# Optimization experiments

Measured on AMD Instinct MI355X. Metric: run time of the kernel, lower is better.

Reference implementation:

```python
import jax, jax.numpy as jnp
import numpy as np


def setup_inputs() -> dict:
    key = jax.random.key(0)
    k1, k2, k3 = jax.random.split(key, 3)
    B, N, C, K = 4, 8192, 256, 16
    q = jax.random.normal(k1, (B, N, C), dtype=jnp.float32)
    q_pos = jax.random.normal(k2, (B, N, 3), dtype=jnp.float32)
    W = jax.random.normal(k3, (2 * C, C), dtype=jnp.float32) / np.sqrt(2 * C)
    b = jnp.zeros((C,), dtype=jnp.float32)
    return {"q": q, "q_pos": q_pos, "W": W, "b": b, "k": K}


def _square_distance(src, dst):
    # src [B,N,3], dst [B,M,3] -> [B,N,M]
    d = -2.0 * jnp.einsum("bnc,bmc->bnm", src, dst)
    d = d + jnp.sum(src * src, axis=-1)[:, :, None]
    d = d + jnp.sum(dst * dst, axis=-1)[:, None, :]
    return d


def reference(q, q_pos, W, b, k):
    # self-attention path: v = q, v_pos = q_pos
    v, v_pos = q, q_pos
    sqrdists = _square_distance(q_pos, v_pos)           # [B,N,M]
    _, idx = jax.lax.top_k(-sqrdists, k)                # k smallest -> [B,N,k]
    # gather neighbors: local_v[b,n,j] = v[b, idx[b,n,j]]
    local_v = jax.vmap(lambda vv, ii: vv[ii])(v, idx)   # [B,N,k,C]
    qk = jnp.broadcast_to(q[:, :, None, :], local_v.shape)
    feature = jnp.concatenate([local_v - qk, qk], axis=-1)  # [B,N,k,2C]
    h = jnp.einsum("bnkf,fc->bnkc", feature, W) + b
    h = jax.nn.leaky_relu(h, negative_slope=0.2)
    out = jnp.max(h, axis=-2)                           # [B,N,C]
    return out
```

## Files before the change

kernel.cpp:

```cpp
#include <hip/hip_runtime.h>
#include <hip/hip_bf16.h>
#include <cstdint>
#include <cstddef>

#define BATCH 4
#define NPT   8192
#define CH    256
#define KNN   16
#define BN_TOT (BATCH * NPT)
#define NSLICE 16
#define SLICE  (NPT / NSLICE)
#define CAP    32
#define MINI   32

typedef __attribute__((ext_vector_type(8))) short bf16x8;
typedef __attribute__((ext_vector_type(4))) float f32x4;

__device__ __forceinline__ float dist2np(const float4 qp, const float4 cp) {
#pragma clang fp contract(off)
  float acc = qp.x * cp.x;
  acc = __builtin_fmaf(qp.y, cp.y, acc);
  acc = __builtin_fmaf(qp.z, cp.z, acc);
  float t = -2.0f * acc;
  t = t + qp.w;
  t = t + cp.w;
  return t;
}

__device__ __forceinline__ unsigned int pk_bf16(float a, float b) {
  __hip_bfloat162 h = __float22bfloat162_rn(make_float2(a, b));
  return *(unsigned int*)&h;
}

__global__ __launch_bounds__(256) void prep_kernel(
    const float* __restrict__ q_pos, const float* __restrict__ W,
    float4* __restrict__ cpack, unsigned short* __restrict__ WbT)
{
  int t = blockIdx.x * 256 + threadIdx.x;
  {
    int k = t >> 9;
    int j = t & 511;
    float v;
    if (j < 256) {
      v = W[k * 256 + j];
    } else {
      int c = j - 256;
      v = W[(256 + k) * 256 + c] - W[k * 256 + c];
    }
    __hip_bfloat16 hb = __float2bfloat16(v);
    WbT[(size_t)j * 256 + k] = *(unsigned short*)&hb;
  }
  if (t < BN_TOT) {
#pragma clang fp contract(off)
    float x = q_pos[3 * t + 0];
    float y = q_pos[3 * t + 1];
    float z = q_pos[3 * t + 2];
    float px = x * x;
    float py = y * y;
    float pz = z * z;
    float s = px + py;
    s = s + pz;
    cpack[t] = make_float4(x, y, z, s);
  }
}

__global__ __launch_bounds__(1024, 8) void knn_kernel(
    const float4* __restrict__ cpack,
    int* __restrict__ idxout)
{
  __shared__ __align__(16) unsigned short cand[NSLICE * 64 * CAP];
  __shared__ unsigned int hist[32][64];
  __shared__ unsigned short scnt[NSLICE][64];
  __shared__ float edge_s[64];
  __shared__ int ubnd[64];

  const int tid = threadIdx.x;
  const int l   = tid & 63;
  const int w   = __builtin_amdgcn_readfirstlane(tid >> 6);
  const int b   = blockIdx.y;
  const int q   = b * NPT + blockIdx.x * 64 + l;

  ((unsigned int*)hist)[tid] = 0u;
  ((unsigned int*)hist)[tid + 1024] = 0u;
  __syncthreads();

  const float4 qp = cpack[q];
  const float m2x = -2.0f * qp.x, m2y = -2.0f * qp.y, m2z = -2.0f * qp.z;
  const float4* __restrict__ cb = cpack + b * NPT;
  const int m0 = w * SLICE;
  unsigned int* hb = (unsigned int*)((char*)&hist[0][0] - (241 << 8)) + l;

#pragma unroll 4
  for (int m = m0; m < m0 + MINI; ++m) {
    float4 cp = cb[m];
    float d = fmaf(m2z, cp.z, fmaf(m2y, cp.y, fmaf(m2x, cp.x, qp.w + cp.w)));
    int r = __float_as_int(d) >> 22;
    r = min(max(r, 241), 272);
    atomicAdd(hb + (r << 6), 1u);
  }
  __syncthreads();

  if (tid < 64) {
    int cum = 0, Bm = 31;
#pragma unroll 1
    for (int bb = 0; bb < 32; ++bb) {
      cum += (int)hist[bb][tid];
      if (cum >= KNN) { Bm = bb; break; }
    }
    ubnd[tid] = 241 + Bm;
  }
  __syncthreads();

  const int ub = ubnd[l];
  const float ubEdgef = __uint_as_float((unsigned)(ub + 1) << 22);
#pragma unroll 8
  for (int m = m0 + MINI; m < m0 + SLICE; ++m) {
    float4 cp = cb[m];
    float d = fmaf(m2z, cp.z, fmaf(m2y, cp.y, fmaf(m2x, cp.x, qp.w + cp.w)));
    if (d < ubEdgef) {
      int r = max(__float_as_int(d) >> 22, 241);
      atomicAdd(hb + (r << 6), 1u);
    }
  }
  __syncthreads();

  if (tid < 64) {
    int cum = 0, B = 31;
#pragma unroll 1
    for (int bb = 0; bb < 32; ++bb) {
      cum += (int)hist[bb][tid];
      if (cum >= KNN) { B = bb; break; }
    }
    edge_s[tid] = __uint_as_float((unsigned)(242 + B) << 22);
  }
  __syncthreads();

  const float edgef = edge_s[l];
  unsigned int cnt = 0;
  unsigned short* mybuf = &cand[(w * 64 + l) * CAP];
#pragma unroll 8
  for (int m = m0; m < m0 + SLICE; ++m) {
    float4 cp = cb[m];
    float d = fmaf(m2z, cp.z, fmaf(m2y, cp.y, fmaf(m2x, cp.x, qp.w + cp.w)));
    if (d < edgef) {
      if (cnt < CAP) mybuf[cnt] = (unsigned short)m;
      cnt++;
    }
  }
  scnt[w][l] = (unsigned short)(cnt < (unsigned)CAP ? cnt : (unsigned)CAP);
  __syncthreads();

  if ((tid >> 6) < 4) {
    const int g = tid >> 6;
    const int nself = (q & (NPT - 1));
    float rd[16]; int ri[16];
#pragma unroll
    for (int j = 0; j < 16; ++j) { rd[j] = __builtin_inff(); ri[j] = nself; }
#pragma unroll 1
    for (int w2 = 4 * g; w2 < 4 * g + 4; ++w2) {
      int cw = (int)scnt[w2][l];
      for (int i = 0; i < cw; ++i) {
        int m = (int)cand[(w2 * 64 + l) * CAP + i];
        float d = dist2np(qp, cb[m]);
        if (d < rd[15]) {
#pragma unroll
          for (int j = 15; j > 0; --j) {
            bool up = d < rd[j - 1];
            float nd = up ? rd[j - 1] : d;
            int   ni = up ? ri[j - 1] : m;
            if (d < rd[j]) { rd[j] = nd; ri[j] = ni; }
          }
          if (d < rd[0]) { rd[0] = d; ri[0] = m; }
        }
      }
    }
    float2* pls = (float2*)(cand + (size_t)g * 8192);
#pragma unroll
    for (int j = 0; j < 16; ++j) {
      int pos = (j + l) & 15;
      pls[l * 16 + pos] = make_float2(rd[j], __int_as_float(ri[j]));
    }
  }
  __syncthreads();

  if (tid < 64) {
    const float2* pls0 = (const float2*)(cand);
    const float2* pls1 = (const float2*)(cand + 8192);
    const float2* pls2 = (const float2*)(cand + 16384);
    const float2* pls3 = (const float2*)(cand + 24576);
    int p0 = 0, p1 = 0, p2 = 0, p3 = 0;
    float2 h0 = pls0[l * 16 + (l & 15)];
    float2 h1 = pls1[l * 16 + (l & 15)];
    float2 h2 = pls2[l * 16 + (l & 15)];
    float2 h3 = pls3[l * 16 + (l & 15)];
#pragma unroll 1
    for (int s = 0; s < 16; ++s) {
      float bd = h0.x; int be = __float_as_int(h0.y); int bg = 0;
      if (h1.x < bd) { bd = h1.x; be = __float_as_int(h1.y); bg = 1; }
      if (h2.x < bd) { bd = h2.x; be = __float_as_int(h2.y); bg = 2; }
      if (h3.x < bd) { bd = h3.x; be = __float_as_int(h3.y); bg = 3; }
      idxout[(size_t)q * 16 + s] = be;
      p0 += (bg == 0); p1 += (bg == 1); p2 += (bg == 2); p3 += (bg == 3);
      int q0 = p0 < 16 ? p0 : 15;
      int q1 = p1 < 16 ? p1 : 15;
      int q2 = p2 < 16 ? p2 : 15;
      int q3 = p3 < 16 ? p3 : 15;
      h0 = pls0[l * 16 + ((q0 + l) & 15)];
      h1 = pls1[l * 16 + ((q1 + l) & 15)];
      h2 = pls2[l * 16 + ((q2 + l) & 15)];
      h3 = pls3[l * 16 + ((q3 + l) & 15)];
    }
  }
}

#define ASTRIDE 40
__global__ __launch_bounds__(256) void gemm_kernel(
    const float* __restrict__ Q, const unsigned short* __restrict__ WbT,
    const float* __restrict__ bias,
    unsigned short* __restrict__ A16, float* __restrict__ Qn)
{
  __shared__ __align__(16) unsigned short As[128 * ASTRIDE];
  __shared__ __align__(16) unsigned short Bs[128 * ASTRIDE];
  const int tid  = threadIdx.x;
  const int lane = tid & 63;
  const int wv   = tid >> 6;
  const int wr   = wv & 1, wc = wv >> 1;
  const int bid  = blockIdx.x;
  const int bm0  = (bid >> 2) * 128;
  const int bn0  = (bid & 3) * 128;
  const int srow = tid >> 1;
  const int skh  = tid & 1;
  const int quad = lane >> 4;
  const int l15  = lane & 15;

  f32x4 acc[4][4];
#pragma unroll
  for (int i = 0; i < 4; ++i)
#pragma unroll
    for (int j = 0; j < 4; ++j) acc[i][j] = (f32x4)0.0f;

  const float* ag = Q + (size_t)(bm0 + srow) * 256 + skh * 16;
  const unsigned short* bg = WbT + (size_t)(bn0 + srow) * 256 + skh * 16;
  unsigned short* asw = &As[srow * ASTRIDE + skh * 16];
  unsigned short* bsw = &Bs[srow * ASTRIDE + skh * 16];

  for (int k0 = 0; k0 < 256; k0 += 32) {
    float4 f0 = *(const float4*)(ag + k0);
    float4 f1 = *(const float4*)(ag + k0 + 4);
    float4 f2 = *(const float4*)(ag + k0 + 8);
    float4 f3 = *(const float4*)(ag + k0 + 12);
    uint4 bv0 = *(const uint4*)(bg + k0);
    uint4 bv1 = *(const uint4*)(bg + k0 + 8);
    uint4 a0, a1;
    a0.x = pk_bf16(f0.x, f0.y); a0.y = pk_bf16(f0.z, f0.w);
    a0.z = pk_bf16(f1.x, f1.y); a0.w = pk_bf16(f1.z, f1.w);
    a1.x = pk_bf16(f2.x, f2.y); a1.y = pk_bf16(f2.z, f2.w);
    a1.z = pk_bf16(f3.x, f3.y); a1.w = pk_bf16(f3.z, f3.w);
    __syncthreads();
    *(uint4*)(asw) = a0;
    *(uint4*)(asw + 8) = a1;
    *(uint4*)(bsw) = bv0;
    *(uint4*)(bsw + 8) = bv1;
    __syncthreads();

    bf16x8 af[4], bf[4];
#pragma unroll
    for (int rt = 0; rt < 4; ++rt)
      af[rt] = *(const bf16x8*)&As[(wr * 64 + rt * 16 + l15) * ASTRIDE + quad * 8];
#pragma unroll
    for (int ct = 0; ct < 4; ++ct)
      bf[ct] = *(const bf16x8*)&Bs[(wc * 64 + ct * 16 + l15) * ASTRIDE + quad * 8];
#pragma unroll
    for (int rt = 0; rt < 4; ++rt)
#pragma unroll
      for (int ct = 0; ct < 4; ++ct)
        acc[rt][ct] = __builtin_amdgcn_mfma_f32_16x16x32_bf16(af[rt], bf[ct], acc[rt][ct], 0, 0, 0);
  }

  if (bn0 < 256) {
#pragma unroll
    for (int ct = 0; ct < 4; ++ct) {
      int col = bn0 + wc * 64 + ct * 16 + l15;
#pragma unroll
      for (int rt = 0; rt < 4; ++rt) {
        int rowb = bm0 + wr * 64 + rt * 16 + quad * 4;
#pragma unroll
        for (int r = 0; r < 4; ++r) {
          __hip_bfloat16 hb = __float2bfloat16(acc[rt][ct][r]);
          A16[(size_t)(rowb + r) * 256 + col] = *(unsigned short*)&hb;
        }
      }
    }
  } else {
#pragma unroll
    for (int ct = 0; ct < 4; ++ct) {
      int col = bn0 + wc * 64 + ct * 16 + l15 - 256;
      float bvl = bias[col];
#pragma unroll
      for (int rt = 0; rt < 4; ++rt) {
        int rowb = bm0 + wr * 64 + rt * 16 + quad * 4;
#pragma unroll
        for (int r = 0; r < 4; ++r)
          Qn[(size_t)(rowb + r) * 256 + col] = acc[rt][ct][r] + bvl;
      }
    }
  }
}

__global__ __launch_bounds__(256) void gather_kernel(
    const unsigned short* __restrict__ A16, const int* __restrict__ idxout,
    float* __restrict__ Out)
{
  __shared__ int sidx[16];
  const int q = blockIdx.x;
  const int b = q >> 13;
  const int c = threadIdx.x;
  if (c < 16) sidx[c] = idxout[(size_t)q * 16 + c];
  __syncthreads();
  const float qn = Out[(size_t)q * 256 + c];
  const unsigned short* __restrict__ Ab = A16 + (size_t)b * NPT * 256;
  float best = -__builtin_inff();
#pragma unroll
  for (int j = 0; j < 16; ++j) {
    unsigned short raw = Ab[(size_t)sidx[j] * 256 + c];
    float a = __uint_as_float((unsigned)raw << 16);
    float h = a + qn;
    best = fmaxf(best, fmaxf(h, 0.2f * h));
  }
  Out[(size_t)q * 256 + c] = best;
}

extern "C" void kernel_launch(void* const* d_in, const int* in_sizes, int n_in,
                              void* d_out, int out_size, void* d_ws, size_t ws_size,
                              hipStream_t stream)
{
  (void)in_sizes; (void)n_in; (void)out_size; (void)ws_size;
  const float* qf   = (const float*)d_in[0];
  const float* qpos = (const float*)d_in[1];
  const float* W    = (const float*)d_in[2];
  const float* bias = (const float*)d_in[3];

  char* ws = (char*)d_ws;
  size_t off = 0;
  auto alloc = [&](size_t bytes) {
    void* p = ws + off;
    off += (bytes + 255) & ~(size_t)255;
    return p;
  };
  float4* cpack       = (float4*)alloc((size_t)BN_TOT * sizeof(float4));
  unsigned short* WbT = (unsigned short*)alloc((size_t)512 * 256 * 2);
  int* idxout         = (int*)alloc((size_t)BN_TOT * KNN * sizeof(int));
  unsigned short* A16 = (unsigned short*)alloc((size_t)BN_TOT * CH * 2);
  float* Out          = (float*)d_out;

  prep_kernel<<<512, 256, 0, stream>>>(qpos, W, cpack, WbT);
  knn_kernel<<<dim3(128, BATCH), 1024, 0, stream>>>(cpack, idxout);
  gemm_kernel<<<1024, 256, 0, stream>>>(qf, WbT, bias, A16, Out);
  gather_kernel<<<BN_TOT, 256, 0, stream>>>(A16, idxout, Out);
}
```

Baseline: 288.4 us.

## Collect KNN candidates during histogram pass and vectorize neighbor gather

The KNN kernel now records candidate indices below the coarse upper bound while it builds the histogram. The third full scan of the slice then runs only when that buffer overflowed. This drops one pass over the slice in the common case, at the cost of extra buffer writes in the second pass. Separately, the gather kernel handles four queries per block and loads four channels per thread with ushort4/float4, which cuts the block count and the number of memory transactions.

```diff
diff --git a/kernel.cpp b/kernel.cpp
--- a/kernel.cpp
+++ b/kernel.cpp
@@ -113,11 +113,24 @@
 
   const int ub = ubnd[l];
   const float ubEdgef = __uint_as_float((unsigned)(ub + 1) << 22);
-#pragma unroll 8
+  unsigned int cnt = 0;
+  unsigned short* mybuf = &cand[(w * 64 + l) * CAP];
+#pragma unroll 4
+  for (int m = m0; m < m0 + MINI; ++m) {
+    float4 cp = cb[m];
+    float d = fmaf(m2z, cp.z, fmaf(m2y, cp.y, fmaf(m2x, cp.x, qp.w + cp.w)));
+    if (d < ubEdgef) {
+      if (cnt < CAP) mybuf[cnt] = (unsigned short)m;
+      cnt++;
+    }
+  }
+#pragma unroll 4
   for (int m = m0 + MINI; m < m0 + SLICE; ++m) {
     float4 cp = cb[m];
     float d = fmaf(m2z, cp.z, fmaf(m2y, cp.y, fmaf(m2x, cp.x, qp.w + cp.w)));
     if (d < ubEdgef) {
+      if (cnt < CAP) mybuf[cnt] = (unsigned short)m;
+      cnt++;
       int r = max(__float_as_int(d) >> 22, 241);
       atomicAdd(hb + (r << 6), 1u);
     }
@@ -135,16 +148,17 @@
   }
   __syncthreads();
 
-  const float edgef = edge_s[l];
-  unsigned int cnt = 0;
-  unsigned short* mybuf = &cand[(w * 64 + l) * CAP];
-#pragma unroll 8
-  for (int m = m0; m < m0 + SLICE; ++m) {
-    float4 cp = cb[m];
-    float d = fmaf(m2z, cp.z, fmaf(m2y, cp.y, fmaf(m2x, cp.x, qp.w + cp.w)));
-    if (d < edgef) {
-      if (cnt < CAP) mybuf[cnt] = (unsigned short)m;
-      cnt++;
+  if (cnt > (unsigned)CAP) {
+    const float edgef = edge_s[l];
+    cnt = 0;
+#pragma unroll 2
+    for (int m = m0; m < m0 + SLICE; ++m) {
+      float4 cp = cb[m];
+      float d = fmaf(m2z, cp.z, fmaf(m2y, cp.y, fmaf(m2x, cp.x, qp.w + cp.w)));
+      if (d < edgef) {
+        if (cnt < CAP) mybuf[cnt] = (unsigned short)m;
+        cnt++;
+      }
     }
   }
   scnt[w][l] = (unsigned short)(cnt < (unsigned)CAP ? cnt : (unsigned)CAP);
@@ -311,23 +325,35 @@
     const unsigned short* __restrict__ A16, const int* __restrict__ idxout,
     float* __restrict__ Out)
 {
-  __shared__ int sidx[16];
-  const int q = blockIdx.x;
-  const int b = q >> 13;
-  const int c = threadIdx.x;
-  if (c < 16) sidx[c] = idxout[(size_t)q * 16 + c];
-  __syncthreads();
-  const float qn = Out[(size_t)q * 256 + c];
-  const unsigned short* __restrict__ Ab = A16 + (size_t)b * NPT * 256;
-  float best = -__builtin_inff();
+  __shared__ int sidx[64];
+  const int tid  = threadIdx.x;
+  const int q0   = blockIdx.x * 4;
+  const int sub  = tid >> 6;
+  const int lane = tid & 63;
+  const int q    = q0 + sub;
+  const int b    = q >> 13;
+  if (tid < 64) sidx[tid] = idxout[(size_t)q0 * 16 + tid];
+  __syncthreads();
+  const int c4 = lane * 4;
+  float* op = Out + (size_t)q * 256 + c4;
+  const float4 qn = *(const float4*)op;
+  const unsigned short* __restrict__ Ab = A16 + (size_t)b * NPT * 256 + c4;
+  const float NI = -__builtin_inff();
+  float4 best = make_float4(NI, NI, NI, NI);
 #pragma unroll
   for (int j = 0; j < 16; ++j) {
-    unsigned short raw = Ab[(size_t)sidx[j] * 256 + c];
-    float a = __uint_as_float((unsigned)raw << 16);
-    float h = a + qn;
-    best = fmaxf(best, fmaxf(h, 0.2f * h));
-  }
-  Out[(size_t)q * 256 + c] = best;
+    const ushort4 raw = *(const ushort4*)(Ab + (size_t)sidx[sub * 16 + j] * 256);
+    float4 h;
+    h.x = __uint_as_float((unsigned)raw.x << 16) + qn.x;
+    h.y = __uint_as_float((unsigned)raw.y << 16) + qn.y;
+    h.z = __uint_as_float((unsigned)raw.z << 16) + qn.z;
+    h.w = __uint_as_float((unsigned)raw.w << 16) + qn.w;
+    best.x = fmaxf(best.x, fmaxf(h.x, 0.2f * h.x));
+    best.y = fmaxf(best.y, fmaxf(h.y, 0.2f * h.y));
+    best.z = fmaxf(best.z, fmaxf(h.z, 0.2f * h.z));
+    best.w = fmaxf(best.w, fmaxf(h.w, 0.2f * h.w));
+  }
+  *(float4*)op = best;
 }
 
 extern "C" void kernel_launch(void* const* d_in, const int* in_sizes, int n_in,
@@ -356,5 +382,5 @@
   prep_kernel<<<512, 256, 0, stream>>>(qpos, W, cpack, WbT);
   knn_kernel<<<dim3(128, BATCH), 1024, 0, stream>>>(cpack, idxout);
   gemm_kernel<<<1024, 256, 0, stream>>>(qf, WbT, bias, A16, Out);
-  gather_kernel<<<BN_TOT, 256, 0, stream>>>(A16, idxout, Out);
-}
+  gather_kernel<<<BN_TOT / 4, 256, 0, stream>>>(A16, idxout, Out);
+}
```

New measurement: 345.6 us. 19.8% more time.
